# Performance work log

Hardware: AMD Instinct MI355X
Metric: run time of the kernel (lower is better)

Reference implementation:

```python
import math
import jax, jax.numpy as jnp
import numpy as np

D_MODEL = 1024
D_FF = 4096
NUM_EXPERTS = 8
TOP_K = 2
CAP_FACTOR = 1.0
AUX_COEF = 0.01
Z_COEF = 0.0


def setup_inputs() -> dict:
    key = jax.random.key(0)
    ks = jax.random.split(key, 6)
    x = jax.random.normal(ks[0], (4, 2048, D_MODEL), dtype=jnp.float32)
    router_w = jax.random.normal(ks[1], (D_MODEL, NUM_EXPERTS), dtype=jnp.float32) / math.sqrt(D_MODEL)
    router_b = jnp.zeros((NUM_EXPERTS,), dtype=jnp.float32)
    w1 = jax.random.normal(ks[2], (NUM_EXPERTS, D_MODEL, D_FF), dtype=jnp.float32) / math.sqrt(D_MODEL)
    w3 = jax.random.normal(ks[3], (NUM_EXPERTS, D_MODEL, D_FF), dtype=jnp.float32) / math.sqrt(D_MODEL)
    w2 = jax.random.normal(ks[4], (NUM_EXPERTS, D_FF, D_MODEL), dtype=jnp.float32) / math.sqrt(D_FF)
    return {"x": x, "router_w": router_w, "router_b": router_b, "w1": w1, "w3": w3, "w2": w2}


def reference(x, router_w, router_b, w1, w3, w2):
    b, s, d = x.shape
    E, k = NUM_EXPERTS, TOP_K
    T = b * s
    x_flat = x.reshape(T, d)

    # ---- router ----
    logits = x_flat @ router_w + router_b                      # [T, E]
    logits_f32 = logits.astype(jnp.float32)
    probs = jax.nn.softmax(logits_f32, axis=-1)                # [T, E]
    topk_p, topk_i = jax.lax.top_k(probs, k)                   # [T, k]
    topk_p = topk_p / jnp.clip(topk_p.sum(-1, keepdims=True), 1e-9)  # normalize_gates
    gate = topk_p.reshape(-1)                                  # [T*k]
    expert_idx = topk_i.reshape(-1)                            # [T*k]

    # ---- aux loss (load balance + z-loss) ----
    importance = probs.mean(axis=0)                            # [E]
    load = jnp.bincount(topk_i[:, 0], length=E).astype(jnp.float32) / T
    lb_loss = (importance * load).sum() * float(E)
    z_loss = jnp.mean(jnp.square(jax.nn.logsumexp(logits_f32, axis=-1)))
    aux_loss = (AUX_COEF * lb_loss + Z_COEF * z_loss).astype(x.dtype)

    # ---- capacity-based dispatch ----
    N = T * k
    cap = max(1, int(math.ceil(CAP_FACTOR * N / E)))
    x_rep = jnp.repeat(x_flat, k, axis=0)                      # [N, d]
    order = jnp.argsort(expert_idx)                            # stable sort by expert
    e_sorted = expert_idx[order]
    x_sorted = x_rep[order]
    g_sorted = gate[order].astype(x.dtype)
    counts = jnp.bincount(e_sorted, length=E)
    starts = jnp.concatenate([jnp.zeros((1,), counts.dtype), jnp.cumsum(counts)[:-1]])
    pos = jnp.arange(N, dtype=counts.dtype) - starts[e_sorted]   # rank within expert group
    keep = pos < cap
    slot = jnp.where(keep, e_sorted * cap + pos, E * cap)      # dropped tokens -> dump row

    buf = jnp.zeros((E * cap + 1, d), dtype=x.dtype).at[slot].set(x_sorted)
    buf = buf[: E * cap].reshape(E, cap, d)                    # [E, C, d]

    # ---- grouped SwiGLU experts ----
    h = jax.nn.silu(jnp.einsum('ecd,edf->ecf', buf, w1)) * jnp.einsum('ecd,edf->ecf', buf, w3)
    y = jnp.einsum('ecf,efd->ecd', h, w2).reshape(E * cap, d)

    # ---- combine ----
    gathered = y[jnp.minimum(slot, E * cap - 1)]
    out_sorted = jnp.where(keep[:, None], gathered, 0.0) * g_sorted[:, None]
    inv = jnp.argsort(order)
    out = out_sorted[inv].reshape(T, k, d).sum(axis=1)
    return out.reshape(b, s, d), aux_loss
```

## Files before the change

### kernel.cpp

```cpp
#include <hip/hip_runtime.h>
#include <hip/hip_bf16.h>
#include <math.h>

constexpr int kT    = 8192;
constexpr int kD    = 1024;
constexpr int kF    = 4096;
constexpr int kE    = 8;
constexpr int kN    = kT * 2;
constexpr int kCap  = 2048;
constexpr int kECap = kE * kCap;

typedef __attribute__((ext_vector_type(8))) short bf16x8;
typedef __attribute__((ext_vector_type(4))) float f32x4;

__device__ __forceinline__ void gload16(const __hip_bfloat16* g, __hip_bfloat16* l) {
  auto gp = (const __attribute__((address_space(1))) __hip_bfloat16*)g;
  auto lp = (__attribute__((address_space(3))) __hip_bfloat16*)l;
  __builtin_amdgcn_global_load_lds((const __attribute__((address_space(1))) void*)gp,
                                   (__attribute__((address_space(3))) void*)lp,
                                   16, 0, 0);
}

#define SYNC_VM(N) do { __builtin_amdgcn_sched_barrier(0); \
  asm volatile("s_waitcnt vmcnt(" #N ")" ::: "memory"); \
  __builtin_amdgcn_s_barrier(); \
  asm volatile("" ::: "memory"); } while (0)

__global__ void init_kernel(int* token_of) {
  int i = blockIdx.x * 256 + threadIdx.x;
  if (i < kECap) token_of[i] = -1;
}

__global__ __launch_bounds__(256)
void transpose64_kernel(const float* __restrict__ srcA, const float* __restrict__ srcB,
                        __hip_bfloat16* __restrict__ dstA, __hip_bfloat16* __restrict__ dstB,
                        int R, int C) {
  __shared__ float tile[64][65];
  const int zz = blockIdx.z;
  const int e = zz & 7;
  const float* src = (zz < 8) ? srcA : srcB;
  __hip_bfloat16* dst = (zz < 8) ? dstA : dstB;
  const size_t mat = (size_t)R * C;
  const float* s = src + (size_t)e * mat;
  __hip_bfloat16* d = dst + (size_t)e * mat;
  const int c0 = blockIdx.x * 64, r0 = blockIdx.y * 64;
  const int tid = threadIdx.x;

  const int lr = tid >> 4, lc4 = (tid & 15) * 4;
#pragma unroll
  for (int p = 0; p < 4; ++p) {
    int r = p * 16 + lr;
    float4 v = *(const float4*)(s + (size_t)(r0 + r) * C + c0 + lc4);
    tile[r][lc4] = v.x; tile[r][lc4 + 1] = v.y; tile[r][lc4 + 2] = v.z; tile[r][lc4 + 3] = v.w;
  }
  __syncthreads();

  const int c = tid >> 2, rc = (tid & 3) * 16;
  union { __hip_bfloat16 h[16]; bf16x8 v[2]; } o;
#pragma unroll
  for (int i = 0; i < 16; ++i) o.h[i] = __float2bfloat16(tile[rc + i][c]);
  __hip_bfloat16* drow = d + (size_t)(c0 + c) * R + r0 + rc;
  *(bf16x8*)drow = o.v[0];
  *(bf16x8*)(drow + 8) = o.v[1];
}

__global__ __launch_bounds__(256)
void router_kernel(const float* __restrict__ x, const float* __restrict__ rw,
                   const float* __restrict__ rb, int* __restrict__ e_idx,
                   float* __restrict__ gates, float* __restrict__ probs_out) {
  int t = blockIdx.x * 4 + (threadIdx.x >> 6);
  int lane = threadIdx.x & 63;
  const float* xr = x + (size_t)t * kD;
  float acc[8];
#pragma unroll
  for (int e = 0; e < 8; ++e) acc[e] = 0.f;
  for (int i = 0; i < kD / 256; ++i) {
    int d = i * 256 + lane * 4;
    float4 xv = *(const float4*)(xr + d);
#pragma unroll
    for (int j = 0; j < 4; ++j) {
      float xs = (j == 0) ? xv.x : (j == 1) ? xv.y : (j == 2) ? xv.z : xv.w;
      const float4* w4 = (const float4*)(rw + (size_t)(d + j) * 8);
      float4 wa = w4[0], wb = w4[1];
      acc[0] += xs * wa.x; acc[1] += xs * wa.y; acc[2] += xs * wa.z; acc[3] += xs * wa.w;
      acc[4] += xs * wb.x; acc[5] += xs * wb.y; acc[6] += xs * wb.z; acc[7] += xs * wb.w;
    }
  }
#pragma unroll
  for (int off = 32; off >= 1; off >>= 1) {
#pragma unroll
    for (int e = 0; e < 8; ++e) acc[e] += __shfl_xor(acc[e], off);
  }
  if (lane == 0) {
    float l[8], m = -1e30f;
#pragma unroll
    for (int e = 0; e < 8; ++e) { l[e] = acc[e] + rb[e]; m = fmaxf(m, l[e]); }
    float p[8], s = 0.f;
#pragma unroll
    for (int e = 0; e < 8; ++e) { p[e] = __expf(l[e] - m); s += p[e]; }
    float inv = 1.f / s;
#pragma unroll
    for (int e = 0; e < 8; ++e) p[e] *= inv;
    int i1 = 0;
#pragma unroll
    for (int e = 1; e < 8; ++e) if (p[e] > p[i1]) i1 = e;
    int i2 = (i1 == 0) ? 1 : 0;
#pragma unroll
    for (int e = 0; e < 8; ++e) if (e != i1 && e != i2 && p[e] > p[i2]) i2 = e;
    float den = fmaxf(p[i1] + p[i2], 1e-9f);
    e_idx[2 * t] = i1; e_idx[2 * t + 1] = i2;
    gates[2 * t] = p[i1] / den; gates[2 * t + 1] = p[i2] / den;
    float4* po = (float4*)(probs_out + (size_t)t * 8);
    po[0] = make_float4(p[0], p[1], p[2], p[3]);
    po[1] = make_float4(p[4], p[5], p[6], p[7]);
  }
}

__global__ __launch_bounds__(1024)
void aux_kernel(const float* __restrict__ probs, const int* __restrict__ e_idx,
                float* __restrict__ aux_out) {
  int tid = threadIdx.x, lane = tid & 63, wave = tid >> 6;
  float imp[8];
  int cnt[8];
#pragma unroll
  for (int e = 0; e < 8; ++e) { imp[e] = 0.f; cnt[e] = 0; }
  for (int t = tid; t < kT; t += 1024) {
    const float4* p4 = (const float4*)(probs + (size_t)t * 8);
    float4 a = p4[0], b = p4[1];
    imp[0] += a.x; imp[1] += a.y; imp[2] += a.z; imp[3] += a.w;
    imp[4] += b.x; imp[5] += b.y; imp[6] += b.z; imp[7] += b.w;
    ++cnt[e_idx[2 * t] & 7];
  }
#pragma unroll
  for (int off = 32; off >= 1; off >>= 1) {
#pragma unroll
    for (int e = 0; e < 8; ++e) {
      imp[e] += __shfl_xor(imp[e], off);
      cnt[e] += __shfl_xor(cnt[e], off);
    }
  }
  __shared__ float simp[16][8];
  __shared__ int scnt[16][8];
  if (lane == 0) {
#pragma unroll
    for (int e = 0; e < 8; ++e) { simp[wave][e] = imp[e]; scnt[wave][e] = cnt[e]; }
  }
  __syncthreads();
  if (tid == 0) {
    float lb = 0.f;
    for (int e = 0; e < 8; ++e) {
      float I = 0.f; int C = 0;
      for (int w = 0; w < 16; ++w) { I += simp[w][e]; C += scnt[w][e]; }
      lb += (I / (float)kT) * ((float)C / (float)kT);
    }
    aux_out[0] = 0.01f * lb * (float)kE;
  }
}

__global__ __launch_bounds__(256)
void rank_kernel(const int* __restrict__ e_idx, int* __restrict__ pos) {
  int e = blockIdx.x;
  __shared__ int wave_sum[4];
  __shared__ int running;
  int tid = threadIdx.x, lane = tid & 63, wave = tid >> 6;
  if (tid == 0) running = 0;
  __syncthreads();
  for (int base = 0; base < kN; base += 256) {
    int i = base + tid;
    bool f = (e_idx[i] == e);
    unsigned long long m = __ballot(f);
    int wpre = __popcll(m & ((1ull << lane) - 1ull));
    if (lane == 0) wave_sum[wave] = __popcll(m);
    __syncthreads();
    int woff = 0;
    for (int w = 0; w < wave; ++w) woff += wave_sum[w];
    int r = running;
    if (f) pos[i] = r + woff + wpre;
    __syncthreads();
    if (tid == 0) running = r + wave_sum[0] + wave_sum[1] + wave_sum[2] + wave_sum[3];
    __syncthreads();
  }
}

__global__ __launch_bounds__(256)
void scatter_kernel(const int* __restrict__ e_idx, const int* __restrict__ pos,
                    int* __restrict__ slot_of, int* __restrict__ token_of) {
  int i = blockIdx.x * 256 + threadIdx.x;
  if (i >= kN) return;
  int p = pos[i];
  if (p < kCap) {
    int slot = e_idx[i] * kCap + p;
    slot_of[i] = slot;
    token_of[slot] = i >> 1;
  } else {
    slot_of[i] = -1;
  }
}

struct __attribute__((aligned(8))) bf16x4s { __hip_bfloat16 v[4]; };

__global__ __launch_bounds__(64)
void gather_kernel(const float* __restrict__ x, const int* __restrict__ token_of,
                   __hip_bfloat16* __restrict__ buf) {
  int slot = blockIdx.x, lane = threadIdx.x;
  int t = token_of[slot];
  __hip_bfloat16* br = buf + (size_t)slot * kD;
  if (t >= 0) {
    const float* xr = x + (size_t)t * kD;
#pragma unroll
    for (int j = 0; j < 4; ++j) {
      int dd = (j * 64 + lane) * 4;
      float4 v = *(const float4*)(xr + dd);
      bf16x4s o;
      o.v[0] = __float2bfloat16(v.x); o.v[1] = __float2bfloat16(v.y);
      o.v[2] = __float2bfloat16(v.z); o.v[3] = __float2bfloat16(v.w);
      *(bf16x4s*)(br + dd) = o;
    }
  } else {
    bf16x4s z;
    z.v[0] = z.v[1] = z.v[2] = z.v[3] = __float2bfloat16(0.f);
#pragma unroll
    for (int j = 0; j < 4; ++j) *(bf16x4s*)(br + (j * 64 + lane) * 4) = z;
  }
}

__global__ __launch_bounds__(512, 2)
void gemm1_kernel(const __hip_bfloat16* __restrict__ Abase,
                  const __hip_bfloat16* __restrict__ W1t,
                  const __hip_bfloat16* __restrict__ W3t,
                  __hip_bfloat16* __restrict__ H) {
  constexpr int K = kD;
  constexpr int NT = K / 64;
  const int e = blockIdx.z, mt = blockIdx.y, ft = blockIdx.x;
  const int tid = threadIdx.x, lane = tid & 63, wave = tid >> 6;
  const int wr = wave >> 1, wc = wave & 1;
  const int frow = lane & 15, fk = lane >> 4;

  const __hip_bfloat16* A  = Abase + (size_t)(e * kCap + mt * 256) * K;
  const __hip_bfloat16* B1 = W1t + ((size_t)e * kF + ft * 128) * K;
  const __hip_bfloat16* B3 = W3t + ((size_t)e * kF + ft * 128) * K;

  extern __shared__ __hip_bfloat16 lds[];

  f32x4 accU[4][4], accV[4][4];
#pragma unroll
  for (int m = 0; m < 4; ++m)
#pragma unroll
    for (int n = 0; n < 4; ++n) {
      accU[m][n] = (f32x4){0.f, 0.f, 0.f, 0.f};
      accV[m][n] = (f32x4){0.f, 0.f, 0.f, 0.f};
    }

  auto stageA = [&](int t, int b) {
#pragma unroll
    for (int j = 0; j < 4; ++j) {
      int c = j * 128 + wc * 64 + lane;
      int rl = c >> 3, s = c & 7;
      const __hip_bfloat16* g = A + (size_t)(wr * 64 + rl) * K + t * 64 + (s ^ (rl & 7)) * 8;
      gload16(g, &lds[b * 32768 + wr * 4096 + (j * 128 + wc * 64) * 8]);
    }
  };
  auto stageB1 = [&](int t, int b) {
#pragma unroll
    for (int j = 0; j < 2; ++j) {
      int c = j * 256 + wr * 64 + lane;
      int rl = c >> 3, s = c & 7;
      const __hip_bfloat16* g = B1 + (size_t)(wc * 64 + rl) * K + t * 64 + (s ^ (rl & 7)) * 8;
      gload16(g, &lds[b * 32768 + 16384 + wc * 4096 + (j * 256 + wr * 64) * 8]);
    }
  };
  auto stageB3 = [&](int t, int b) {
#pragma unroll
    for (int j = 0; j < 2; ++j) {
      int c = j * 256 + wr * 64 + lane;
      int rl = c >> 3, s = c & 7;
      const __hip_bfloat16* g = B3 + (size_t)(wc * 64 + rl) * K + t * 64 + (s ^ (rl & 7)) * 8;
      gload16(g, &lds[b * 32768 + 16384 + 8192 + wc * 4096 + (j * 256 + wr * 64) * 8]);
    }
  };
  auto phase = [&](int b, f32x4 (&ac)[4][4], bf16x8 (&af)[4][2], int broff, bool loadA) {
    if (loadA) {
#pragma unroll
      for (int m = 0; m < 4; ++m)
#pragma unroll
        for (int h = 0; h < 2; ++h) {
          int row = wr * 64 + m * 16 + frow;
          af[m][h] = *(const bf16x8*)&lds[b * 32768 + row * 64 + ((h * 4 + fk) ^ (row & 7)) * 8];
        }
    }
    bf16x8 bf[4][2];
#pragma unroll
    for (int n = 0; n < 4; ++n)
#pragma unroll
      for (int h = 0; h < 2; ++h) {
        int row = broff + wc * 64 + n * 16 + frow;
        bf[n][h] = *(const bf16x8*)&lds[b * 32768 + 16384 + row * 64 + ((h * 4 + fk) ^ (row & 7)) * 8];
      }
    __builtin_amdgcn_s_setprio(1);
#pragma unroll
    for (int m = 0; m < 4; ++m)
#pragma unroll
      for (int n = 0; n < 4; ++n)
#pragma unroll
        for (int h = 0; h < 2; ++h)
          ac[m][n] = __builtin_amdgcn_mfma_f32_16x16x32_bf16(af[m][h], bf[n][h], ac[m][n], 0, 0, 0);
    __builtin_amdgcn_s_setprio(0);
    __builtin_amdgcn_sched_barrier(0);
  };

  stageA(0, 0); stageB1(0, 0); stageB3(0, 0);

  for (int t = 0; t < NT; ++t) {
    const int b = t & 1, nb = b ^ 1;
    const bool nx = (t + 1 < NT);
    SYNC_VM(2);
    if (nx) stageA(t + 1, nb);
    bf16x8 af[4][2];
    phase(b, accU, af, 0, true);
    if (nx) { SYNC_VM(4); } else { SYNC_VM(0); }
    if (nx) stageB1(t + 1, nb);
    phase(b, accV, af, 128, false);
    if (nx) stageB3(t + 1, nb);
  }

  __hip_bfloat16* Ht = H + (size_t)(e * kCap + mt * 256) * kF + ft * 128;
#pragma unroll
  for (int m = 0; m < 4; ++m)
#pragma unroll
    for (int n = 0; n < 4; ++n)
#pragma unroll
      for (int r = 0; r < 4; ++r) {
        int row = wr * 64 + m * 16 + fk * 4 + r;
        int col = wc * 64 + n * 16 + frow;
        float u = accU[m][n][r], v = accV[m][n][r];
        float hval = (u / (1.f + __expf(-u))) * v;
        Ht[(size_t)row * kF + col] = __float2bfloat16(hval);
      }
}

__global__ __launch_bounds__(512, 2)
void gemm2_kernel(const __hip_bfloat16* __restrict__ Hbase,
                  const __hip_bfloat16* __restrict__ W2t,
                  float* __restrict__ Y) {
  constexpr int K = kF;
  constexpr int NT = K / 64;
  const int e = blockIdx.z, mt = blockIdx.y, nt = blockIdx.x;
  const int tid = threadIdx.x, lane = tid & 63, wave = tid >> 6;
  const int wr = wave >> 2, wc = wave & 3;
  const int frow = lane & 15, fk = lane >> 4;

  const __hip_bfloat16* A = Hbase + (size_t)(e * kCap + mt * 256) * K;
  const __hip_bfloat16* B = W2t + ((size_t)e * kD + nt * 256) * K;

  extern __shared__ __hip_bfloat16 lds[];

  f32x4 acc[2][4][4];
#pragma unroll
  for (int p = 0; p < 2; ++p)
#pragma unroll
    for (int m = 0; m < 4; ++m)
#pragma unroll
      for (int n = 0; n < 4; ++n) acc[p][m][n] = (f32x4){0.f, 0.f, 0.f, 0.f};

  auto stageB = [&](int t, int b) {
#pragma unroll
    for (int j = 0; j < 4; ++j) {
      int c = j * 128 + wr * 64 + lane;
      int rl = c >> 3, s = c & 7;
      const __hip_bfloat16* g = B + (size_t)(wc * 64 + rl) * K + t * 64 + (s ^ (rl & 7)) * 8;
      gload16(g, &lds[b * 32768 + 16384 + wc * 4096 + (j * 128 + wr * 64) * 8]);
    }
  };
  auto stageA = [&](int t, int p, int b) {
    int q = 2 * wr + p;
#pragma unroll
    for (int j = 0; j < 2; ++j) {
      int c = j * 256 + wc * 64 + lane;
      int rl = c >> 3, s = c & 7;
      const __hip_bfloat16* g = A + (size_t)(q * 64 + rl) * K + t * 64 + (s ^ (rl & 7)) * 8;
      gload16(g, &lds[b * 32768 + q * 4096 + (j * 256 + wc * 64) * 8]);
    }
  };
  auto phase = [&](int b, int p, f32x4 (&ac)[4][4], bf16x8 (&bf)[4][2], bool loadB) {
    bf16x8 a[4][2];
#pragma unroll
    for (int m = 0; m < 4; ++m)
#pragma unroll
      for (int h = 0; h < 2; ++h) {
        int row = wr * 128 + p * 64 + m * 16 + frow;
        a[m][h] = *(const bf16x8*)&lds[b * 32768 + row * 64 + ((h * 4 + fk) ^ (row & 7)) * 8];
      }
    if (loadB) {
#pragma unroll
      for (int n = 0; n < 4; ++n)
#pragma unroll
        for (int h = 0; h < 2; ++h) {
          int row = wc * 64 + n * 16 + frow;
          bf[n][h] = *(const bf16x8*)&lds[b * 32768 + 16384 + row * 64 + ((h * 4 + fk) ^ (row & 7)) * 8];
        }
    }
    __builtin_amdgcn_s_setprio(1);
#pragma unroll
    for (int m = 0; m < 4; ++m)
#pragma unroll
      for (int n = 0; n < 4; ++n)
#pragma unroll
        for (int h = 0; h < 2; ++h)
          ac[m][n] = __builtin_amdgcn_mfma_f32_16x16x32_bf16(a[m][h], bf[n][h], ac[m][n], 0, 0, 0);
    __builtin_amdgcn_s_setprio(0);
    __builtin_amdgcn_sched_barrier(0);
  };

  stageB(0, 0); stageA(0, 0, 0); stageA(0, 1, 0);

  for (int t = 0; t < NT; ++t) {
    const int b = t & 1, nb = b ^ 1;
    const bool nx = (t + 1 < NT);
    SYNC_VM(2);
    if (nx) stageB(t + 1, nb);
    bf16x8 bf[4][2];
    phase(b, 0, acc[0], bf, true);
    if (nx) { SYNC_VM(4); } else { SYNC_VM(0); }
    if (nx) stageA(t + 1, 0, nb);
    phase(b, 1, acc[1], bf, false);
    if (nx) stageA(t + 1, 1, nb);
  }

  float* Yt = Y + (size_t)(e * kCap + mt * 256) * kD + nt * 256;
#pragma unroll
  for (int p = 0; p < 2; ++p)
#pragma unroll
    for (int m = 0; m < 4; ++m)
#pragma unroll
      for (int n = 0; n < 4; ++n)
#pragma unroll
        for (int r = 0; r < 4; ++r) {
          int row = wr * 128 + p * 64 + m * 16 + fk * 4 + r;
          int col = wc * 64 + n * 16 + frow;
          Yt[(size_t)row * kD + col] = acc[p][m][n][r];
        }
}

__global__ __launch_bounds__(256)
void combine_kernel(const float* __restrict__ Y, const int* __restrict__ slot_of,
                    const float* __restrict__ gates, float* __restrict__ out) {
  int t = blockIdx.x;
  int dd = threadIdx.x * 4;
  int s0 = slot_of[2 * t], s1 = slot_of[2 * t + 1];
  float g0 = gates[2 * t], g1 = gates[2 * t + 1];
  float4 r = {0.f, 0.f, 0.f, 0.f};
  if (s0 >= 0) {
    float4 v = *(const float4*)(Y + (size_t)s0 * kD + dd);
    r.x += g0 * v.x; r.y += g0 * v.y; r.z += g0 * v.z; r.w += g0 * v.w;
  }
  if (s1 >= 0) {
    float4 v = *(const float4*)(Y + (size_t)s1 * kD + dd);
    r.x += g1 * v.x; r.y += g1 * v.y; r.z += g1 * v.z; r.w += g1 * v.w;
  }
  *(float4*)(out + (size_t)t * kD + dd) = r;
}

extern "C" void kernel_launch(void* const* d_in, const int* in_sizes, int n_in,
                              void* d_out, int out_size, void* d_ws, size_t ws_size,
                              hipStream_t stream) {
  (void)in_sizes; (void)n_in; (void)out_size; (void)ws_size;
  const float* x  = (const float*)d_in[0];
  const float* rw = (const float*)d_in[1];
  const float* rb = (const float*)d_in[2];
  const float* w1 = (const float*)d_in[3];
  const float* w3 = (const float*)d_in[4];
  const float* w2 = (const float*)d_in[5];
  float* out = (float*)d_out;

  char* base = (char*)d_ws;
  size_t off = 0;
  auto alloc = [&](size_t bytes) -> char* {
    char* r = base + off;
    off += (bytes + 255) & ~(size_t)255;
    return r;
  };
  __hip_bfloat16* w1t = (__hip_bfloat16*)alloc((size_t)kE * kF * kD * 2);
  __hip_bfloat16* w3t = (__hip_bfloat16*)alloc((size_t)kE * kF * kD * 2);
  __hip_bfloat16* w2t = (__hip_bfloat16*)alloc((size_t)kE * kD * kF * 2);
  __hip_bfloat16* buf = (__hip_bfloat16*)alloc((size_t)kECap * kD * 2);
  __hip_bfloat16* h   = (__hip_bfloat16*)alloc((size_t)kECap * kF * 2);
  float*          y   = (float*)alloc((size_t)kECap * kD * 4);
  int*   e_idx    = (int*)alloc((size_t)kN * 4);
  float* gates    = (float*)alloc((size_t)kN * 4);
  int*   pos      = (int*)alloc((size_t)kN * 4);
  int*   slot_of  = (int*)alloc((size_t)kN * 4);
  int*   token_of = (int*)alloc((size_t)kECap * 4);
  float* probs    = (float*)alloc((size_t)kT * 8 * 4);

  init_kernel<<<kECap / 256, 256, 0, stream>>>(token_of);
  router_kernel<<<kT / 4, 256, 0, stream>>>(x, rw, rb, e_idx, gates, probs);
  aux_kernel<<<1, 1024, 0, stream>>>(probs, e_idx, out + (size_t)kT * kD);
  rank_kernel<<<kE, 256, 0, stream>>>(e_idx, pos);
  scatter_kernel<<<kN / 256, 256, 0, stream>>>(e_idx, pos, slot_of, token_of);
  gather_kernel<<<kECap, 64, 0, stream>>>(x, token_of, buf);
  transpose64_kernel<<<dim3(kF / 64, kD / 64, 16), 256, 0, stream>>>(w1, w3, w1t, w3t, kD, kF);
  gemm1_kernel<<<dim3(kF / 128, kCap / 256, kE), 512, 131072, stream>>>(buf, w1t, w3t, h);
  transpose64_kernel<<<dim3(kD / 64, kF / 64, 8), 256, 0, stream>>>(w2, w2, w2t, w2t, kF, kD);
  gemm2_kernel<<<dim3(kD / 256, kCap / 256, kE), 512, 131072, stream>>>(h, w2t, y);
  combine_kernel<<<kT, 256, 0, stream>>>(y, slot_of, gates, out);
}
```

Baseline: 612.6 us.

## Restructure gemm2 into four-phase pipeline with block barriers and cooperative staging

Rewrites the second expert GEMM's main loop as four quarter phases, each computing a 4x2 fragment block. Global-to-LDS staging is spread across the phases and issued by all 512 threads cooperatively, and the A tile for step t+2 is prefetched early. Explicit workgroup barriers and lgkmcnt waits now sit around each phase. The aim is to overlap loads with MFMA more evenly and to cut per-wave register pressure from holding B fragments. In exchange it adds many more barriers per iteration, which could stall waves.

New measurement: 622.0 us. No clear change (+1.5%).

```diff
diff --git a/kernel.cpp b/kernel.cpp
--- a/kernel.cpp
+++ b/kernel.cpp
@@ -338,6 +338,39 @@
       }
 }
 
+#define G2_PHASE(MH, NH, STAGE_STMT)                                          \
+  {                                                                           \
+    bf16x8 a[4][2], bb[2][2];                                                 \
+    _Pragma("unroll") for (int m = 0; m < 4; ++m)                             \
+      _Pragma("unroll") for (int h = 0; h < 2; ++h) {                         \
+        int row = wr * 128 + (MH) * 64 + m * 16 + frow;                       \
+        a[m][h] = *(const bf16x8*)&lds[b * 32768 + row * 64 +                 \
+                                       ((h * 4 + fk) ^ (row & 7)) * 8];       \
+      }                                                                       \
+    _Pragma("unroll") for (int n = 0; n < 2; ++n)                             \
+      _Pragma("unroll") for (int h = 0; h < 2; ++h) {                         \
+        int row = wc * 64 + (NH) * 32 + n * 16 + frow;                        \
+        bb[n][h] = *(const bf16x8*)&lds[b * 32768 + 16384 + row * 64 +        \
+                                        ((h * 4 + fk) ^ (row & 7)) * 8];      \
+      }                                                                       \
+    STAGE_STMT;                                                               \
+    __builtin_amdgcn_sched_barrier(0);                                        \
+    __builtin_amdgcn_s_barrier();                                             \
+    asm volatile("s_waitcnt lgkmcnt(0)" ::: "memory");                        \
+    __builtin_amdgcn_sched_barrier(0);                                        \
+    __builtin_amdgcn_s_setprio(1);                                            \
+    _Pragma("unroll") for (int m = 0; m < 4; ++m)                             \
+      _Pragma("unroll") for (int n = 0; n < 2; ++n)                           \
+        _Pragma("unroll") for (int h = 0; h < 2; ++h)                         \
+          acc[(MH) * 4 + m][(NH) * 2 + n] =                                   \
+              __builtin_amdgcn_mfma_f32_16x16x32_bf16(                        \
+                  a[m][h], bb[n][h], acc[(MH) * 4 + m][(NH) * 2 + n], 0, 0, 0); \
+    __builtin_amdgcn_s_setprio(0);                                            \
+    __builtin_amdgcn_sched_barrier(0);                                        \
+    __builtin_amdgcn_s_barrier();                                             \
+    __builtin_amdgcn_sched_barrier(0);                                        \
+  }
+
 __global__ __launch_bounds__(512, 2)
 void gemm2_kernel(const __hip_bfloat16* __restrict__ Hbase,
                   const __hip_bfloat16* __restrict__ W2t,
@@ -354,91 +387,55 @@
 
   extern __shared__ __hip_bfloat16 lds[];
 
-  f32x4 acc[2][4][4];
-#pragma unroll
-  for (int p = 0; p < 2; ++p)
-#pragma unroll
-    for (int m = 0; m < 4; ++m)
-#pragma unroll
-      for (int n = 0; n < 4; ++n) acc[p][m][n] = (f32x4){0.f, 0.f, 0.f, 0.f};
-
-  auto stageB = [&](int t, int b) {
-#pragma unroll
-    for (int j = 0; j < 4; ++j) {
-      int c = j * 128 + wr * 64 + lane;
+  f32x4 acc[8][4];
+#pragma unroll
+  for (int m = 0; m < 8; ++m)
+#pragma unroll
+    for (int n = 0; n < 4; ++n) acc[m][n] = (f32x4){0.f, 0.f, 0.f, 0.f};
+
+  auto stg = [&](const __hip_bfloat16* gbase, int rowbase, int t, int ldsbase) {
+#pragma unroll
+    for (int j = 0; j < 2; ++j) {
+      int c = j * 512 + tid;
       int rl = c >> 3, s = c & 7;
-      const __hip_bfloat16* g = B + (size_t)(wc * 64 + rl) * K + t * 64 + (s ^ (rl & 7)) * 8;
-      gload16(g, &lds[b * 32768 + 16384 + wc * 4096 + (j * 128 + wr * 64) * 8]);
+      const __hip_bfloat16* g = gbase + (size_t)(rowbase + rl) * K + t * 64 + (s ^ (rl & 7)) * 8;
+      gload16(g, &lds[ldsbase + (j * 512 + wave * 64) * 8]);
     }
   };
-  auto stageA = [&](int t, int p, int b) {
-    int q = 2 * wr + p;
-#pragma unroll
-    for (int j = 0; j < 2; ++j) {
-      int c = j * 256 + wc * 64 + lane;
-      int rl = c >> 3, s = c & 7;
-      const __hip_bfloat16* g = A + (size_t)(q * 64 + rl) * K + t * 64 + (s ^ (rl & 7)) * 8;
-      gload16(g, &lds[b * 32768 + q * 4096 + (j * 256 + wc * 64) * 8]);
-    }
-  };
-  auto phase = [&](int b, int p, f32x4 (&ac)[4][4], bf16x8 (&bf)[4][2], bool loadB) {
-    bf16x8 a[4][2];
-#pragma unroll
-    for (int m = 0; m < 4; ++m)
-#pragma unroll
-      for (int h = 0; h < 2; ++h) {
-        int row = wr * 128 + p * 64 + m * 16 + frow;
-        a[m][h] = *(const bf16x8*)&lds[b * 32768 + row * 64 + ((h * 4 + fk) ^ (row & 7)) * 8];
-      }
-    if (loadB) {
-#pragma unroll
-      for (int n = 0; n < 4; ++n)
-#pragma unroll
-        for (int h = 0; h < 2; ++h) {
-          int row = wc * 64 + n * 16 + frow;
-          bf[n][h] = *(const bf16x8*)&lds[b * 32768 + 16384 + row * 64 + ((h * 4 + fk) ^ (row & 7)) * 8];
-        }
-    }
-    __builtin_amdgcn_s_setprio(1);
-#pragma unroll
-    for (int m = 0; m < 4; ++m)
-#pragma unroll
-      for (int n = 0; n < 4; ++n)
-#pragma unroll
-        for (int h = 0; h < 2; ++h)
-          ac[m][n] = __builtin_amdgcn_mfma_f32_16x16x32_bf16(a[m][h], bf[n][h], ac[m][n], 0, 0, 0);
-    __builtin_amdgcn_s_setprio(0);
-    __builtin_amdgcn_sched_barrier(0);
-  };
-
-  stageB(0, 0); stageA(0, 0, 0); stageA(0, 1, 0);
+
+  stg(A, 0, 0, 0);
+  stg(A, 128, 0, 8192);
+  stg(B, 0, 0, 16384);
+  stg(B, 128, 0, 24576);
+  stg(A, 0, 1, 32768);
 
   for (int t = 0; t < NT; ++t) {
     const int b = t & 1, nb = b ^ 1;
-    const bool nx = (t + 1 < NT);
-    SYNC_VM(2);
-    if (nx) stageB(t + 1, nb);
-    bf16x8 bf[4][2];
-    phase(b, 0, acc[0], bf, true);
-    if (nx) { SYNC_VM(4); } else { SYNC_VM(0); }
-    if (nx) stageA(t + 1, 0, nb);
-    phase(b, 1, acc[1], bf, false);
-    if (nx) stageA(t + 1, 1, nb);
+    const bool m1 = (t + 1 < NT), m2 = (t + 2 < NT);
+    __builtin_amdgcn_sched_barrier(0);
+    if (m1) { asm volatile("s_waitcnt vmcnt(2)" ::: "memory"); }
+    else    { asm volatile("s_waitcnt vmcnt(0)" ::: "memory"); }
+    __builtin_amdgcn_s_barrier();
+    __builtin_amdgcn_sched_barrier(0);
+
+    G2_PHASE(0, 0, if (m1) stg(A, 128, t + 1, nb * 32768 + 8192));
+    G2_PHASE(0, 1, if (m1) stg(B, 0, t + 1, nb * 32768 + 16384));
+    G2_PHASE(1, 0, if (m1) stg(B, 128, t + 1, nb * 32768 + 24576));
+    G2_PHASE(1, 1, );
+    if (m2) stg(A, 0, t + 2, b * 32768);
   }
 
   float* Yt = Y + (size_t)(e * kCap + mt * 256) * kD + nt * 256;
 #pragma unroll
-  for (int p = 0; p < 2; ++p)
-#pragma unroll
-    for (int m = 0; m < 4; ++m)
-#pragma unroll
-      for (int n = 0; n < 4; ++n)
-#pragma unroll
-        for (int r = 0; r < 4; ++r) {
-          int row = wr * 128 + p * 64 + m * 16 + fk * 4 + r;
-          int col = wc * 64 + n * 16 + frow;
-          Yt[(size_t)row * kD + col] = acc[p][m][n][r];
-        }
+  for (int m = 0; m < 8; ++m)
+#pragma unroll
+    for (int n = 0; n < 4; ++n)
+#pragma unroll
+      for (int r = 0; r < 4; ++r) {
+        int row = wr * 128 + m * 16 + fk * 4 + r;
+        int col = wc * 64 + n * 16 + frow;
+        Yt[(size_t)row * kD + col] = acc[m][n][r];
+      }
 }
 
 __global__ __launch_bounds__(256)
```
